# Optimization experiments

Hardware: AMD Instinct MI355X
Metric: run time of the kernel (lower is better)

Reference implementation:

```python
import jax, jax.numpy as jnp
import numpy as np

N0, N1, N2 = 400000, 100000, 25000   # nodes per scale (finest -> coarsest)
E0, E1, E2 = 1600000, 400000, 100000
HID, OUT = 64, 2
STATIC_D, DYN_D = 6, 10
K = 3  # filter-matrix polynomial order
NUM_SCALES = 3


def setup_inputs() -> dict:
    key = jax.random.key(0)
    ks = jax.random.split(key, 20)
    def nrm(k, shape, scale=1.0):
        return jax.random.normal(k, shape, dtype=jnp.float32) * scale
    Ntot = N0 + N1 + N2
    inp = {}
    inp["static_features"] = nrm(ks[0], (Ntot, STATIC_D))
    inp["dynamic_features"] = nrm(ks[1], (Ntot, DYN_D))
    Es, Ns = [E0, E1, E2], [N0, N1, N2]
    for i in range(NUM_SCALES):
        inp[f"edge_index{i}"] = jax.random.randint(ks[2 + i], (2, Es[i]), 0, Ns[i], dtype=jnp.int32)
        inp[f"edge_attr{i}"] = jax.random.uniform(ks[5 + i], (Es[i],), dtype=jnp.float32)
    inp["pool_idx1"] = jax.random.randint(ks[8], (N1,), 0, N0, dtype=jnp.int32)
    inp["pool_idx2"] = jax.random.randint(ks[9], (N2,), 0, N0, dtype=jnp.int32)
    fin = STATIC_D + DYN_D
    inp["enc_W1"] = nrm(ks[10], (fin, HID), 1.0 / np.sqrt(fin))
    inp["enc_b1"] = jnp.zeros((HID,), jnp.float32)
    inp["enc_W2"] = nrm(ks[11], (HID, HID), 1.0 / np.sqrt(HID))
    inp["enc_b2"] = jnp.zeros((HID,), jnp.float32)
    inp["enc_prelu"] = jnp.float32(0.25)
    inp["gcn_W"] = nrm(ks[12], (NUM_SCALES, HID, HID), 1.0 / np.sqrt(HID))
    inp["gcn_b"] = jnp.zeros((NUM_SCALES, HID), jnp.float32)
    inp["filter_matrix"] = jnp.ones((NUM_SCALES, K), jnp.float32)
    inp["dec_W1"] = nrm(ks[13], (HID, HID), 1.0 / np.sqrt(HID))
    inp["dec_b1"] = jnp.zeros((HID,), jnp.float32)
    inp["dec_W2"] = nrm(ks[14], (HID, OUT), 1.0 / np.sqrt(HID))
    inp["dec_b2"] = jnp.zeros((OUT,), jnp.float32)
    inp["dec_prelu"] = jnp.float32(0.25)
    return inp


def prelu(x, a):
    return jnp.where(x > 0, x, a * x)


def gcn_conv(x, W, b, src, dst, ew, n):
    # PyG GCNConv: linear, then symmetric-normalized propagation with self loops (weight 1), then bias.
    h = x @ W
    deg = jnp.zeros((n,), x.dtype).at[dst].add(ew) + 1.0  # +1 for self loop
    dinv = jax.lax.rsqrt(deg)
    norm = dinv[src] * ew * dinv[dst]                      # [E]
    out = jnp.zeros_like(h).at[dst].add(norm[:, None] * h[src])
    out = out + h * (dinv * dinv)[:, None]                 # self-loop term: 1/deg
    return out + b


def scatter_mean(x, idx, n):
    cnt = jnp.zeros((n,), x.dtype).at[idx].add(1.0)
    s = jnp.zeros((n, x.shape[1]), x.dtype).at[idx].add(x)
    return s / jnp.maximum(cnt, 1.0)[:, None]


def reference(static_features, dynamic_features, edge_index0, edge_attr0,
              edge_index1, edge_attr1, edge_index2, edge_attr2,
              pool_idx1, pool_idx2,
              enc_W1, enc_b1, enc_W2, enc_b2, enc_prelu,
              gcn_W, gcn_b, filter_matrix,
              dec_W1, dec_b1, dec_W2, dec_b2, dec_prelu):
    # Encoder MLP (prelu after every layer, shared prelu param per MLP)
    x = jnp.concatenate([static_features, dynamic_features], -1)
    x = prelu(x @ enc_W1 + enc_b1, enc_prelu)
    x = prelu(x @ enc_W2 + enc_b2, enc_prelu)

    # Split into scales (node_ptr is static)
    ptr = [0, N0, N0 + N1, N0 + N1 + N2]
    xs = [x[ptr[i]:ptr[i + 1]] for i in range(NUM_SCALES)]
    eis = [edge_index0, edge_index1, edge_index2]
    eas = [edge_attr0, edge_attr1, edge_attr2]
    Ns = [N0, N1, N2]

    # MSGNN layers: K repeated (conv -> tanh), mixed by filter_matrix
    outs = []
    for i in range(NUM_SCALES):
        src, dst = eis[i][0], eis[i][1]
        h = xs[i]
        acc = jnp.zeros_like(h)
        for k in range(K):
            h = jnp.tanh(gcn_conv(h, gcn_W[i], gcn_b[i], src, dst, eas[i], Ns[i]))
            acc = acc + filter_matrix[i, k] * h
        outs.append(acc)

    # Skip-connection pooling: scatter-mean coarse scales onto finest scale
    fin = outs[0]
    fin = fin + scatter_mean(outs[1], pool_idx1, N0)
    fin = fin + scatter_mean(outs[2], pool_idx2, N0)

    # Decoder MLP
    y = prelu(fin @ dec_W1 + dec_b1, dec_prelu)
    y = prelu(y @ dec_W2 + dec_b2, dec_prelu)
    return y
```

## Files before the change

kernel.cpp:

```cpp
#include <hip/hip_runtime.h>
#include <hip/hip_bf16.h>

typedef __hip_bfloat16 bf16;
typedef short  bf16x8  __attribute__((ext_vector_type(8)));
typedef __bf16 bf16x8n __attribute__((ext_vector_type(8)));
typedef float  f32x4   __attribute__((ext_vector_type(4)));

constexpr int cN0 = 400000, cN1 = 100000, cN2 = 25000;
constexpr int cNTOT = cN0 + cN1 + cN2;
constexpr int cE0 = 1600000, cE1 = 400000, cE2 = 100000;

static __device__ __forceinline__ float b2f(bf16 x) { return __bfloat162float(x); }

static __device__ __forceinline__ short f2bf_rtne(float f) {
    unsigned u = __float_as_uint(f);
    u = (u + 0x7fffu + ((u >> 16) & 1u)) >> 16;
    return (short)u;
}
static __device__ __forceinline__ void split2(float x, short& h, short& l) {
    unsigned u = __float_as_uint(x);
    h = (short)(u >> 16);
    l = f2bf_rtne(x - __uint_as_float(u & 0xffff0000u));
}

static __device__ __forceinline__ f32x4 mfma16(bf16x8 a, bf16x8 b, f32x4 c) {
    return __builtin_amdgcn_mfma_f32_16x16x32_bf16((bf16x8n)a, (bf16x8n)b, c, 0, 0, 0);
}

static __device__ __forceinline__ void pack_a8(const float* s8, bf16x8& ah, bf16x8& al) {
    float4 v0 = ((const float4*)s8)[0];
    float4 v1 = ((const float4*)s8)[1];
    float xx[8] = {v0.x, v0.y, v0.z, v0.w, v1.x, v1.y, v1.z, v1.w};
#pragma unroll
    for (int j = 0; j < 8; j++) { short h, l; split2(xx[j], h, l); ah[j] = h; al[j] = l; }
}

static __device__ __forceinline__ void pack_b8(const float* __restrict__ W, int ldn,
                                               int kbase, int col, int kmax,
                                               bf16x8& bh, bf16x8& bl) {
#pragma unroll
    for (int j = 0; j < 8; j++) {
        int k = kbase + j;
        float w = (k < kmax) ? W[(size_t)k * ldn + col] : 0.f;
        short h, l; split2(w, h, l); bh[j] = h; bl[j] = l;
    }
}

__global__ __launch_bounds__(256, 2)
void enc_kernel(const float* __restrict__ stat, const float* __restrict__ dyn,
                const float* __restrict__ W1, const float* __restrict__ b1,
                const float* __restrict__ W2, const float* __restrict__ b2,
                const float* __restrict__ pa, bf16* __restrict__ X, int nn)
{
    __shared__ float sF[4][16 * 20];
    __shared__ float sH[4][16 * 68];
    const int lane = threadIdx.x & 63;
    const int slot = threadIdx.x >> 6;
    const int r = lane & 15, g4 = lane >> 4;
    const int wid = blockIdx.x * (blockDim.x >> 6) + slot;
    const int nw  = gridDim.x * (blockDim.x >> 6);

    bf16x8 B1h[4], B1l[4], B2h[2][4], B2l[2][4];
#pragma unroll
    for (int nb = 0; nb < 4; nb++)
        pack_b8(W1, 64, g4 * 8, nb * 16 + r, 16, B1h[nb], B1l[nb]);
#pragma unroll
    for (int s = 0; s < 2; s++)
#pragma unroll
        for (int nb = 0; nb < 4; nb++)
            pack_b8(W2, 64, s * 32 + g4 * 8, nb * 16 + r, 64, B2h[s][nb], B2l[s][nb]);
    float bc1[4], bc2[4];
#pragma unroll
    for (int nb = 0; nb < 4; nb++) { bc1[nb] = b1[nb * 16 + r]; bc2[nb] = b2[nb * 16 + r]; }
    const float a = pa[0];
    float* F = sF[slot];
    float* H = sH[slot];
    const int ntile = (nn + 15) >> 4;

    for (int tt = wid; tt < ntile; tt += nw) {
        const int n0 = tt << 4;
        const int nv = min(16, nn - n0);
        for (int t = lane; t < nv * 6; t += 64)
            F[(t / 6) * 20 + (t % 6)] = stat[(size_t)n0 * 6 + t];
        for (int t = lane; t < nv * 10; t += 64)
            F[(t / 10) * 20 + 6 + (t % 10)] = dyn[(size_t)n0 * 10 + t];
        __builtin_amdgcn_wave_barrier();

        f32x4 C1[4];
#pragma unroll
        for (int nb = 0; nb < 4; nb++) C1[nb] = (f32x4){bc1[nb], bc1[nb], bc1[nb], bc1[nb]};
        bf16x8 ah, al;
        if (g4 < 2) pack_a8(F + r * 20 + g4 * 8, ah, al);
        else        { ah = (bf16x8)(short)0; al = (bf16x8)(short)0; }
#pragma unroll
        for (int nb = 0; nb < 4; nb++) {
            C1[nb] = mfma16(ah, B1h[nb], C1[nb]);
            C1[nb] = mfma16(ah, B1l[nb], C1[nb]);
            C1[nb] = mfma16(al, B1h[nb], C1[nb]);
        }
#pragma unroll
        for (int nb = 0; nb < 4; nb++)
#pragma unroll
            for (int q = 0; q < 4; q++) {
                float v = C1[nb][q];
                v = v > 0.f ? v : a * v;
                H[(g4 * 4 + q) * 68 + nb * 16 + r] = v;
            }
        __builtin_amdgcn_wave_barrier();

        f32x4 C2[4];
#pragma unroll
        for (int nb = 0; nb < 4; nb++) C2[nb] = (f32x4){bc2[nb], bc2[nb], bc2[nb], bc2[nb]};
#pragma unroll
        for (int s = 0; s < 2; s++) {
            bf16x8 a2h, a2l;
            pack_a8(H + r * 68 + s * 32 + g4 * 8, a2h, a2l);
#pragma unroll
            for (int nb = 0; nb < 4; nb++) {
                C2[nb] = mfma16(a2h, B2h[s][nb], C2[nb]);
                C2[nb] = mfma16(a2h, B2l[s][nb], C2[nb]);
                C2[nb] = mfma16(a2l, B2h[s][nb], C2[nb]);
            }
        }
#pragma unroll
        for (int nb = 0; nb < 4; nb++)
#pragma unroll
            for (int q = 0; q < 4; q++) {
                float v = C2[nb][q];
                v = v > 0.f ? v : a * v;
                const int row = g4 * 4 + q;
                if (row < nv)
                    X[(size_t)(n0 + row) * 64 + nb * 16 + r] = __float2bfloat16(v);
            }
        __builtin_amdgcn_wave_barrier();
    }
}

__global__ void zint_kernel(int* p, int n)   { int t = blockIdx.x * 256 + threadIdx.x; if (t < n) p[t] = 0; }
__global__ void fill1_kernel(float* p, int n){ int t = blockIdx.x * 256 + threadIdx.x; if (t < n) p[t] = 1.f; }
__global__ void degacc_kernel(const int* __restrict__ dst, const float* __restrict__ ew,
                              float* __restrict__ deg, int ne)
{
    int e = blockIdx.x * 256 + threadIdx.x;
    if (e < ne) unsafeAtomicAdd(&deg[dst[e]], ew[e]);
}
__global__ void rsqrt_kernel(float* p, int n){ int t = blockIdx.x * 256 + threadIdx.x; if (t < n) p[t] = rsqrtf(p[t]); }
__global__ void cnt_edge_kernel(const int* __restrict__ dst, int* __restrict__ cnt, int ne)
{
    int e = blockIdx.x * 256 + threadIdx.x;
    if (e < ne) atomicAdd(&cnt[dst[e]], 1);
}

__global__ void scan_blk_kernel(const int* __restrict__ cnt, int* __restrict__ base,
                                int* __restrict__ bsum, int n)
{
    __shared__ int s[256];
    const int tid = threadIdx.x;
    const int t = blockIdx.x * 256 + tid;
    int v = (t < n) ? cnt[t] : 0;
    s[tid] = v;
    __syncthreads();
#pragma unroll
    for (int d = 1; d < 256; d <<= 1) {
        int u = (tid >= d) ? s[tid - d] : 0;
        __syncthreads();
        s[tid] += u;
        __syncthreads();
    }
    if (t < n) base[t] = s[tid] - v;
    if (tid == 255) bsum[blockIdx.x] = s[255];
}
__global__ void scan_top_kernel(int* __restrict__ bsum, int nb)
{
    __shared__ int s[256];
    __shared__ int carry;
    const int tid = threadIdx.x;
    if (tid == 0) carry = 0;
    __syncthreads();
    for (int c0 = 0; c0 < nb; c0 += 256) {
        const int t = c0 + tid;
        int v = (t < nb) ? bsum[t] : 0;
        s[tid] = v;
        __syncthreads();
#pragma unroll
        for (int d = 1; d < 256; d <<= 1) {
            int u = (tid >= d) ? s[tid - d] : 0;
            __syncthreads();
            s[tid] += u;
            __syncthreads();
        }
        if (t < nb) bsum[t] = carry + s[tid] - v;
        __syncthreads();
        if (tid == 255) carry += s[255];
        __syncthreads();
    }
}
__global__ void scan_add_kernel(int* __restrict__ base, const int* __restrict__ bsum,
                                int* __restrict__ cur, int n)
{
    const int t = blockIdx.x * 256 + threadIdx.x;
    if (t < n) { int b = base[t] + bsum[blockIdx.x]; base[t] = b; cur[t] = b; }
}

__global__ void grab_kernel(const int* __restrict__ cnt, int* __restrict__ base,
                            int* __restrict__ cur, int* __restrict__ gc, int n)
{
    int t = blockIdx.x * 256 + threadIdx.x;
    if (t < n) { int b = atomicAdd(gc, cnt[t]); base[t] = b; cur[t] = b; }
}
__global__ void fill_edge_kernel(const int* __restrict__ src, const int* __restrict__ dst,
                                 const float* __restrict__ ew, const float* __restrict__ dinv,
                                 int* __restrict__ cur, int* __restrict__ srcp,
                                 bf16* __restrict__ normp, int ne)
{
    int e = blockIdx.x * 256 + threadIdx.x;
    if (e >= ne) return;
    int d = dst[e], s = src[e];
    int pos = atomicAdd(&cur[d], 1);
    srcp[pos]  = s;
    normp[pos] = __float2bfloat16(dinv[s] * ew[e] * dinv[d]);
}
__global__ void cnt_idx_kernel(const int* __restrict__ idx, int* __restrict__ cnt, int n)
{
    int j = blockIdx.x * 256 + threadIdx.x;
    if (j < n) atomicAdd(&cnt[idx[j]], 1);
}
__global__ void fill_idx_kernel(const int* __restrict__ idx, int* __restrict__ cur,
                                int* __restrict__ jp, int n)
{
    int j = blockIdx.x * 256 + threadIdx.x;
    if (j >= n) return;
    int pos = atomicAdd(&cur[idx[j]], 1);
    jp[pos] = j;
}

__global__ __launch_bounds__(256, 3)
void fused_conv_kernel(const int* __restrict__ base,
                       const int* __restrict__ srcp, const bf16* __restrict__ normp,
                       const bf16* __restrict__ h_in, bf16* __restrict__ h_out,
                       const float* __restrict__ dinv,
                       const float* __restrict__ W, int woff,
                       const float* __restrict__ bias, int boff,
                       const float* __restrict__ filt, int foff,
                       int first, int store_h, float* __restrict__ acc,
                       int nn, int ne)
{
    __shared__ float sb[4][16 * 68];
    const int lane = threadIdx.x & 63;
    const int slot = threadIdx.x >> 6;
    const int r = lane & 15, g4 = lane >> 4;
    const int wid  = blockIdx.x * (blockDim.x >> 6) + slot;
    const int nw   = gridDim.x * (blockDim.x >> 6);

    bf16x8 Bh[2][4], Bl[2][4];
#pragma unroll
    for (int s = 0; s < 2; s++)
#pragma unroll
        for (int nb = 0; nb < 4; nb++)
            pack_b8(W + woff, 64, s * 32 + g4 * 8, nb * 16 + r, 64, Bh[s][nb], Bl[s][nb]);
    float bc[4];
#pragma unroll
    for (int nb = 0; nb < 4; nb++) bc[nb] = bias[boff + nb * 16 + r];
    const float fc = filt[foff];
    float* sbrow = sb[slot];
    const int ngrp = (nn + 15) >> 4;

    for (int grp = wid; grp < ngrp; grp += nw) {
        const int n0 = grp << 4;
        const int idx = n0 + lane;
        int rpl = 0;
        if (lane <= 16) rpl = (idx < nn) ? base[idx] : ne;
        const int rp0 = __shfl(rpl, 0);
        const int rpG = __shfl(rpl, 16);

        int cur = 0;
        int rnext = __shfl(rpl, 1);
        float g = 0.f;

        for (int eb = rp0; eb < rpG; eb += 64) {
            const int cc = min(64, rpG - eb);
            int sv = 0; float nv = 0.f;
            if (lane < cc) {
                sv = srcp[eb + lane];
                nv = b2f(normp[eb + lane]);
            }
            for (int j = 0; j < cc; j += 8) {
                float p[8], m[8];
#pragma unroll
                for (int t = 0; t < 8; t++) {
                    const int jt = min(j + t, cc - 1);
                    const int st = __shfl(sv, jt);
                    const float mt = __shfl(nv, jt);
                    m[t] = (j + t < cc) ? mt : 0.f;
                    p[t] = b2f(h_in[(size_t)st * 64 + lane]);
                }
#pragma unroll
                for (int t = 0; t < 8; t++) {
                    const int je = eb + j + t;
                    while (je >= rnext) {
                        sbrow[cur * 68 + lane] = g;
                        g = 0.f;
                        cur++;
                        rnext = (cur < 16) ? __shfl(rpl, cur + 1) : 0x7fffffff;
                    }
                    g += m[t] * p[t];
                }
            }
        }
        while (cur < 16) {
            sbrow[cur * 68 + lane] = g;
            g = 0.f;
            cur++;
        }
        __builtin_amdgcn_wave_barrier();

        const int nv16 = min(16, nn - n0);
        for (int i = 0; i < nv16; i++) {
            const int n_i = n0 + i;
            const float di = dinv[n_i];
            sbrow[i * 68 + lane] += b2f(h_in[(size_t)n_i * 64 + lane]) * di * di;
        }
        __builtin_amdgcn_wave_barrier();

        f32x4 C[4];
#pragma unroll
        for (int nb = 0; nb < 4; nb++) C[nb] = (f32x4){bc[nb], bc[nb], bc[nb], bc[nb]};
#pragma unroll
        for (int s = 0; s < 2; s++) {
            bf16x8 ah, al;
            pack_a8(sbrow + r * 68 + s * 32 + g4 * 8, ah, al);
#pragma unroll
            for (int nb = 0; nb < 4; nb++) {
                C[nb] = mfma16(ah, Bh[s][nb], C[nb]);
                C[nb] = mfma16(ah, Bl[s][nb], C[nb]);
                C[nb] = mfma16(al, Bh[s][nb], C[nb]);
            }
        }
#pragma unroll
        for (int nb = 0; nb < 4; nb++)
#pragma unroll
            for (int q = 0; q < 4; q++) {
                const int row = g4 * 4 + q;
                if (row < nv16) {
                    const float sv_ = C[nb][q];
                    const float e = __expf(2.f * sv_);
                    const float h = 1.f - 2.f * __builtin_amdgcn_rcpf(e + 1.f);
                    const size_t ai = (size_t)(n0 + row) * 64 + nb * 16 + r;
                    if (store_h) h_out[ai] = __float2bfloat16(h);
                    acc[ai] = (first ? 0.f : acc[ai]) + fc * h;
                }
            }
        __builtin_amdgcn_wave_barrier();
    }
}

__global__ void pool_gather_kernel(const int* __restrict__ base, const int* __restrict__ cnt,
                                   const int* __restrict__ jp, const float* __restrict__ accc,
                                   float* __restrict__ fin, int nn)
{
    const int lane = threadIdx.x & 63;
    const int n = blockIdx.x * (blockDim.x >> 6) + (threadIdx.x >> 6);
    if (n >= nn) return;
    const int m = cnt[n];
    if (m == 0) return;
    const int bs = base[n];
    float s = 0.f;
    for (int t = bs; t < bs + m; t++) {
        int j = jp[t];
        s += accc[(size_t)j * 64 + lane];
    }
    fin[(size_t)n * 64 + lane] += s / (float)m;
}

__global__ __launch_bounds__(256, 3)
void dec_kernel(const float* __restrict__ fin,
                const float* __restrict__ W1, const float* __restrict__ b1,
                const float* __restrict__ W2, const float* __restrict__ b2,
                const float* __restrict__ pa, float* __restrict__ out, int nn)
{
    const int lane = threadIdx.x & 63;
    const int r = lane & 15, g4 = lane >> 4;
    const int wid = blockIdx.x * (blockDim.x >> 6) + (threadIdx.x >> 6);
    const int nw  = gridDim.x * (blockDim.x >> 6);

    bf16x8 Wh[2][4], Wl[2][4];
#pragma unroll
    for (int s = 0; s < 2; s++)
#pragma unroll
        for (int nb = 0; nb < 4; nb++)
            pack_b8(W1, 64, s * 32 + g4 * 8, nb * 16 + r, 64, Wh[s][nb], Wl[s][nb]);
    float bc[4], w20[4], w21[4];
#pragma unroll
    for (int nb = 0; nb < 4; nb++) {
        bc[nb]  = b1[nb * 16 + r];
        w20[nb] = W2[(nb * 16 + r) * 2 + 0];
        w21[nb] = W2[(nb * 16 + r) * 2 + 1];
    }
    const float bb20 = b2[0], bb21 = b2[1];
    const float a = pa[0];
    const int ntile = (nn + 15) >> 4;

    for (int tt = wid; tt < ntile; tt += nw) {
        const int n0 = tt << 4;
        f32x4 C[4];
#pragma unroll
        for (int nb = 0; nb < 4; nb++) C[nb] = (f32x4){bc[nb], bc[nb], bc[nb], bc[nb]};
#pragma unroll
        for (int s = 0; s < 2; s++) {
            bf16x8 ah, al;
            pack_a8(fin + (size_t)(n0 + r) * 64 + s * 32 + g4 * 8, ah, al);
#pragma unroll
            for (int nb = 0; nb < 4; nb++) {
                C[nb] = mfma16(ah, Wh[s][nb], C[nb]);
                C[nb] = mfma16(ah, Wl[s][nb], C[nb]);
                C[nb] = mfma16(al, Wh[s][nb], C[nb]);
            }
        }
#pragma unroll
        for (int q = 0; q < 4; q++) {
            float p0 = 0.f, p1 = 0.f;
#pragma unroll
            for (int nb = 0; nb < 4; nb++) {
                float y = C[nb][q];
                y = y > 0.f ? y : a * y;
                p0 += y * w20[nb]; p1 += y * w21[nb];
            }
            p0 += __shfl_xor(p0, 1); p1 += __shfl_xor(p1, 1);
            p0 += __shfl_xor(p0, 2); p1 += __shfl_xor(p1, 2);
            p0 += __shfl_xor(p0, 4); p1 += __shfl_xor(p1, 4);
            p0 += __shfl_xor(p0, 8); p1 += __shfl_xor(p1, 8);
            if (r == 0) {
                const int node = n0 + g4 * 4 + q;
                if (node < nn) {
                    float o0 = p0 + bb20; o0 = o0 > 0.f ? o0 : a * o0;
                    float o1 = p1 + bb21; o1 = o1 > 0.f ? o1 : a * o1;
                    ((float2*)out)[node] = make_float2(o0, o1);
                }
            }
        }
    }
}

extern "C" void kernel_launch(void* const* d_in, const int* in_sizes, int n_in,
                              void* d_out, int out_size, void* d_ws, size_t ws_size,
                              hipStream_t stream)
{
    const float* stat = (const float*)d_in[0];
    const float* dyn  = (const float*)d_in[1];
    const int*   ei[3]   = {(const int*)d_in[2], (const int*)d_in[4], (const int*)d_in[6]};
    const float* ea[3]   = {(const float*)d_in[3], (const float*)d_in[5], (const float*)d_in[7]};
    const int*   pidx[2] = {(const int*)d_in[8], (const int*)d_in[9]};
    const float* encW1 = (const float*)d_in[10]; const float* encb1 = (const float*)d_in[11];
    const float* encW2 = (const float*)d_in[12]; const float* encb2 = (const float*)d_in[13];
    const float* encpa = (const float*)d_in[14];
    const float* gW    = (const float*)d_in[15]; const float* gbias = (const float*)d_in[16];
    const float* filt  = (const float*)d_in[17];
    const float* dW1   = (const float*)d_in[18]; const float* db1   = (const float*)d_in[19];
    const float* dW2   = (const float*)d_in[20]; const float* db2   = (const float*)d_in[21];
    const float* dpa   = (const float*)d_in[22];

    auto al = [](size_t x) { return (x + 255) & ~(size_t)255; };
    char* w = (char*)d_ws;
    size_t off = 0;
    bf16* X    = (bf16*)(w + off); off += al((size_t)cNTOT * 64 * 2);
    bf16* HB   = (bf16*)(w + off); off += al((size_t)cN0 * 64 * 2);
    float* FIN = (float*)(w + off); off += al((size_t)cN0 * 64 * 4);
    float* ACCC= (float*)(w + off); off += al((size_t)cN1 * 64 * 4);
    float* DINV= (float*)(w + off); off += al((size_t)cN0 * 4);
    int* CNTI  = (int*)(w + off);  off += al((size_t)cN0 * 4);
    int* BASE  = (int*)(w + off);  off += al((size_t)cN0 * 4);
    int* CUR   = (int*)(w + off);  off += al((size_t)cN0 * 4);
    int* SRCP  = (int*)(w + off);  off += al((size_t)cE0 * 4);
    bf16* NORMP= (bf16*)(w + off); off += al((size_t)cE0 * 2);
    int* JP    = (int*)(w + off);  off += al((size_t)cN1 * 4);
    int* GC    = (int*)(w + off);  off += 256;
    int* BSUM  = (int*)(w + off);  off += al((size_t)2048 * 4);

    const int Ns[3]  = {cN0, cN1, cN2};
    const int Es[3]  = {cE0, cE1, cE2};
    const int ptr[3] = {0, cN0, cN0 + cN1};
#define NB(x) (((x) + 255) / 256)

    enc_kernel<<<4096, 256, 0, stream>>>(stat, dyn, encW1, encb1, encW2, encb2, encpa, X, cNTOT);

    for (int i = 0; i < 3; i++) {
        const int* srcp_in = ei[i];
        const int* dstp    = ei[i] + Es[i];
        fill1_kernel <<<NB(Ns[i]), 256, 0, stream>>>(DINV, Ns[i]);
        degacc_kernel<<<NB(Es[i]), 256, 0, stream>>>(dstp, ea[i], DINV, Es[i]);
        rsqrt_kernel <<<NB(Ns[i]), 256, 0, stream>>>(DINV, Ns[i]);
        zint_kernel    <<<NB(Ns[i]), 256, 0, stream>>>(CNTI, Ns[i]);
        cnt_edge_kernel<<<NB(Es[i]), 256, 0, stream>>>(dstp, CNTI, Es[i]);
        scan_blk_kernel<<<NB(Ns[i]), 256, 0, stream>>>(CNTI, BASE, BSUM, Ns[i]);
        scan_top_kernel<<<1, 256, 0, stream>>>(BSUM, NB(Ns[i]));
        scan_add_kernel<<<NB(Ns[i]), 256, 0, stream>>>(BASE, BSUM, CUR, Ns[i]);
        fill_edge_kernel<<<NB(Es[i]), 256, 0, stream>>>(srcp_in, dstp, ea[i], DINV, CUR, SRCP, NORMP, Es[i]);

        bf16* ping = X + (size_t)ptr[i] * 64;
        bf16* pong = HB;
        float* acc_i = (i == 0) ? FIN : ACCC;
        for (int k = 0; k < 3; k++) {
            bf16* hin  = (k & 1) ? pong : ping;
            bf16* hout = (k & 1) ? ping : pong;
            fused_conv_kernel<<<4096, 256, 0, stream>>>(BASE, SRCP, NORMP,
                hin, hout, DINV, gW, i * 4096, gbias, i * 64,
                filt, i * 3 + k, (k == 0) ? 1 : 0, (k < 2) ? 1 : 0, acc_i, Ns[i], Es[i]);
        }
        if (i >= 1) {
            int nj = (i == 1) ? cN1 : cN2;
            const int* pp = pidx[i - 1];
            zint_kernel    <<<NB(cN0), 256, 0, stream>>>(CNTI, cN0);
            zint_kernel    <<<1, 256, 0, stream>>>(GC, 1);
            cnt_idx_kernel <<<NB(nj), 256, 0, stream>>>(pp, CNTI, nj);
            grab_kernel    <<<NB(cN0), 256, 0, stream>>>(CNTI, BASE, CUR, GC, cN0);
            fill_idx_kernel<<<NB(nj), 256, 0, stream>>>(pp, CUR, JP, nj);
            pool_gather_kernel<<<(cN0 + 3) / 4, 256, 0, stream>>>(BASE, CNTI, JP, ACCC, FIN, cN0);
        }
    }
    dec_kernel<<<4096, 256, 0, stream>>>(FIN, dW1, db1, dW2, db2, dpa, (float*)d_out, cN0);
#undef NB
}
```

Before: 1.552 ms.

## Restructure edge aggregation into 4-node lane groups and fuse preprocessing kernels

The gather-aggregate loop in the fused conv kernel now splits the wave into four 16-lane groups. Each group handles four destination nodes and each lane loads 4 bf16 features with one 8-byte load, replacing the old scheme of one feature per lane per edge with a shared serial segment walk. The self-loop term is vectorised per row. Preprocessing kernels are fused: init of dinv and counts, degree plus count atomics, rsqrt folded into the block scan, and the two zeroing kernels merged. The conv grid is sized to the number of node groups, which cuts launch count and idle waves but adds some lane divergence from per-group segment flushing.

```diff
diff --git a/kernel.cpp b/kernel.cpp
--- a/kernel.cpp
+++ b/kernel.cpp
@@ -11,6 +11,8 @@
 constexpr int cE0 = 1600000, cE1 = 400000, cE2 = 100000;
 
 static __device__ __forceinline__ float b2f(bf16 x) { return __bfloat162float(x); }
+static __device__ __forceinline__ float bflo(unsigned u) { return __uint_as_float(u << 16); }
+static __device__ __forceinline__ float bfhi(unsigned u) { return __uint_as_float(u & 0xffff0000u); }
 
 static __device__ __forceinline__ short f2bf_rtne(float f) {
     unsigned u = __float_as_uint(f);
@@ -136,23 +138,24 @@
     }
 }
 
-__global__ void zint_kernel(int* p, int n)   { int t = blockIdx.x * 256 + threadIdx.x; if (t < n) p[t] = 0; }
-__global__ void fill1_kernel(float* p, int n){ int t = blockIdx.x * 256 + threadIdx.x; if (t < n) p[t] = 1.f; }
-__global__ void degacc_kernel(const int* __restrict__ dst, const float* __restrict__ ew,
-                              float* __restrict__ deg, int ne)
+__global__ void init_scale_kernel(float* dinv, int* cnti, int n)
+{
+    int t = blockIdx.x * 256 + threadIdx.x;
+    if (t < n) { dinv[t] = 1.f; cnti[t] = 0; }
+}
+__global__ void edge_deg_cnt_kernel(const int* __restrict__ dst, const float* __restrict__ ew,
+                                    float* __restrict__ deg, int* __restrict__ cnt, int ne)
 {
     int e = blockIdx.x * 256 + threadIdx.x;
-    if (e < ne) unsafeAtomicAdd(&deg[dst[e]], ew[e]);
-}
-__global__ void rsqrt_kernel(float* p, int n){ int t = blockIdx.x * 256 + threadIdx.x; if (t < n) p[t] = rsqrtf(p[t]); }
-__global__ void cnt_edge_kernel(const int* __restrict__ dst, int* __restrict__ cnt, int ne)
-{
-    int e = blockIdx.x * 256 + threadIdx.x;
-    if (e < ne) atomicAdd(&cnt[dst[e]], 1);
+    if (e < ne) {
+        int d = dst[e];
+        unsafeAtomicAdd(&deg[d], ew[e]);
+        atomicAdd(&cnt[d], 1);
+    }
 }
 
 __global__ void scan_blk_kernel(const int* __restrict__ cnt, int* __restrict__ base,
-                                int* __restrict__ bsum, int n)
+                                int* __restrict__ bsum, float* __restrict__ dinv, int n)
 {
     __shared__ int s[256];
     const int tid = threadIdx.x;
@@ -167,7 +170,10 @@
         s[tid] += u;
         __syncthreads();
     }
-    if (t < n) base[t] = s[tid] - v;
+    if (t < n) {
+        base[t] = s[tid] - v;
+        dinv[t] = rsqrtf(dinv[t]);
+    }
     if (tid == 255) bsum[blockIdx.x] = s[255];
 }
 __global__ void scan_top_kernel(int* __restrict__ bsum, int nb)
@@ -220,6 +226,12 @@
     srcp[pos]  = s;
     normp[pos] = __float2bfloat16(dinv[s] * ew[e] * dinv[d]);
 }
+__global__ void zint2_kernel(int* __restrict__ p, int* __restrict__ gc, int n)
+{
+    int t = blockIdx.x * 256 + threadIdx.x;
+    if (t < n) p[t] = 0;
+    if (t == 0 && blockIdx.x == 0) gc[0] = 0;
+}
 __global__ void cnt_idx_kernel(const int* __restrict__ idx, int* __restrict__ cnt, int n)
 {
     int j = blockIdx.x * 256 + threadIdx.x;
@@ -267,61 +279,79 @@
 
     for (int grp = wid; grp < ngrp; grp += nw) {
         const int n0 = grp << 4;
-        const int idx = n0 + lane;
         int rpl = 0;
-        if (lane <= 16) rpl = (idx < nn) ? base[idx] : ne;
-        const int rp0 = __shfl(rpl, 0);
-        const int rpG = __shfl(rpl, 16);
-
-        int cur = 0;
-        int rnext = __shfl(rpl, 1);
-        float g = 0.f;
-
-        for (int eb = rp0; eb < rpG; eb += 64) {
-            const int cc = min(64, rpG - eb);
-            int sv = 0; float nv = 0.f;
-            if (lane < cc) {
-                sv = srcp[eb + lane];
-                nv = b2f(normp[eb + lane]);
-            }
-            for (int j = 0; j < cc; j += 8) {
-                float p[8], m[8];
-#pragma unroll
-                for (int t = 0; t < 8; t++) {
-                    const int jt = min(j + t, cc - 1);
-                    const int st = __shfl(sv, jt);
-                    const float mt = __shfl(nv, jt);
-                    m[t] = (j + t < cc) ? mt : 0.f;
-                    p[t] = b2f(h_in[(size_t)st * 64 + lane]);
-                }
-#pragma unroll
-                for (int t = 0; t < 8; t++) {
-                    const int je = eb + j + t;
-                    while (je >= rnext) {
-                        sbrow[cur * 68 + lane] = g;
-                        g = 0.f;
-                        cur++;
-                        rnext = (cur < 16) ? __shfl(rpl, cur + 1) : 0x7fffffff;
-                    }
-                    g += m[t] * p[t];
-                }
-            }
-        }
-        while (cur < 16) {
-            sbrow[cur * 68 + lane] = g;
-            g = 0.f;
-            cur++;
-        }
+        if (lane <= 16) rpl = (n0 + lane < nn) ? base[n0 + lane] : ne;
+        const int b4 = g4 << 2;
+        const int q0 = __shfl(rpl, b4);
+        const int q1 = __shfl(rpl, b4 + 1);
+        const int q2 = __shfl(rpl, b4 + 2);
+        const int q3 = __shfl(rpl, b4 + 3);
+        const int q4 = __shfl(rpl, b4 + 4);
+
+        int   curl  = 0;
+        int   rnext = q1;
+        float g0 = 0.f, g1 = 0.f, g2 = 0.f, g3 = 0.f;
+        auto flush = [&]() {
+            *(float4*)(sbrow + (b4 + curl) * 68 + (r << 2)) = make_float4(g0, g1, g2, g3);
+            g0 = g1 = g2 = g3 = 0.f;
+            curl++;
+            rnext = (curl == 1) ? q2 : (curl == 2) ? q3 : (curl == 3) ? q4 : 0x7fffffff;
+        };
+
+        for (int eb = q0; eb < q4; eb += 16) {
+            const int ei_ = min(eb + r, q4 - 1);
+            int   sv = srcp[ei_];
+            float nv = (eb + r < q4) ? b2f(normp[ei_]) : 0.f;
+#pragma unroll
+            for (int t = 0; t < 16; t += 4) {
+                const int bidx = (g4 << 4) + t;
+                int   s0 = __shfl(sv, bidx),     s1 = __shfl(sv, bidx + 1);
+                int   s2 = __shfl(sv, bidx + 2), s3 = __shfl(sv, bidx + 3);
+                float m0 = __shfl(nv, bidx),     m1 = __shfl(nv, bidx + 1);
+                float m2 = __shfl(nv, bidx + 2), m3 = __shfl(nv, bidx + 3);
+                uint2 p0 = *(const uint2*)(h_in + ((size_t)s0 << 6) + (r << 2));
+                uint2 p1 = *(const uint2*)(h_in + ((size_t)s1 << 6) + (r << 2));
+                uint2 p2 = *(const uint2*)(h_in + ((size_t)s2 << 6) + (r << 2));
+                uint2 p3 = *(const uint2*)(h_in + ((size_t)s3 << 6) + (r << 2));
+                while (eb + t     >= rnext) flush();
+                g0 += m0 * bflo(p0.x); g1 += m0 * bfhi(p0.x);
+                g2 += m0 * bflo(p0.y); g3 += m0 * bfhi(p0.y);
+                while (eb + t + 1 >= rnext) flush();
+                g0 += m1 * bflo(p1.x); g1 += m1 * bfhi(p1.x);
+                g2 += m1 * bflo(p1.y); g3 += m1 * bfhi(p1.y);
+                while (eb + t + 2 >= rnext) flush();
+                g0 += m2 * bflo(p2.x); g1 += m2 * bfhi(p2.x);
+                g2 += m2 * bflo(p2.y); g3 += m2 * bfhi(p2.y);
+                while (eb + t + 3 >= rnext) flush();
+                g0 += m3 * bflo(p3.x); g1 += m3 * bfhi(p3.x);
+                g2 += m3 * bflo(p3.y); g3 += m3 * bfhi(p3.y);
+            }
+        }
+        while (curl < 4) flush();
         __builtin_amdgcn_wave_barrier();
 
+        {
+            const int node = n0 + r;
+            const int ncl = min(node, nn - 1);
+            float di = dinv[ncl];
+            di = (node < nn) ? di * di : 0.f;
+            float* rowp = sbrow + r * 68 + (g4 << 4);
+#pragma unroll
+            for (int hh = 0; hh < 2; hh++) {
+                uint4 hv = *(const uint4*)(h_in + ((size_t)ncl << 6) + (g4 << 4) + hh * 8);
+                float4 f0 = *(float4*)(rowp + hh * 8);
+                float4 f1 = *(float4*)(rowp + hh * 8 + 4);
+                f0.x += di * bflo(hv.x); f0.y += di * bfhi(hv.x);
+                f0.z += di * bflo(hv.y); f0.w += di * bfhi(hv.y);
+                f1.x += di * bflo(hv.z); f1.y += di * bfhi(hv.z);
+                f1.z += di * bflo(hv.w); f1.w += di * bfhi(hv.w);
+                *(float4*)(rowp + hh * 8)     = f0;
+                *(float4*)(rowp + hh * 8 + 4) = f1;
+            }
+        }
+        __builtin_amdgcn_wave_barrier();
+
         const int nv16 = min(16, nn - n0);
-        for (int i = 0; i < nv16; i++) {
-            const int n_i = n0 + i;
-            const float di = dinv[n_i];
-            sbrow[i * 68 + lane] += b2f(h_in[(size_t)n_i * 64 + lane]) * di * di;
-        }
-        __builtin_amdgcn_wave_barrier();
-
         f32x4 C[4];
 #pragma unroll
         for (int nb = 0; nb < 4; nb++) C[nb] = (f32x4){bc[nb], bc[nb], bc[nb], bc[nb]};
@@ -486,31 +516,29 @@
     for (int i = 0; i < 3; i++) {
         const int* srcp_in = ei[i];
         const int* dstp    = ei[i] + Es[i];
-        fill1_kernel <<<NB(Ns[i]), 256, 0, stream>>>(DINV, Ns[i]);
-        degacc_kernel<<<NB(Es[i]), 256, 0, stream>>>(dstp, ea[i], DINV, Es[i]);
-        rsqrt_kernel <<<NB(Ns[i]), 256, 0, stream>>>(DINV, Ns[i]);
-        zint_kernel    <<<NB(Ns[i]), 256, 0, stream>>>(CNTI, Ns[i]);
-        cnt_edge_kernel<<<NB(Es[i]), 256, 0, stream>>>(dstp, CNTI, Es[i]);
-        scan_blk_kernel<<<NB(Ns[i]), 256, 0, stream>>>(CNTI, BASE, BSUM, Ns[i]);
-        scan_top_kernel<<<1, 256, 0, stream>>>(BSUM, NB(Ns[i]));
-        scan_add_kernel<<<NB(Ns[i]), 256, 0, stream>>>(BASE, BSUM, CUR, Ns[i]);
-        fill_edge_kernel<<<NB(Es[i]), 256, 0, stream>>>(srcp_in, dstp, ea[i], DINV, CUR, SRCP, NORMP, Es[i]);
+        init_scale_kernel  <<<NB(Ns[i]), 256, 0, stream>>>(DINV, CNTI, Ns[i]);
+        edge_deg_cnt_kernel<<<NB(Es[i]), 256, 0, stream>>>(dstp, ea[i], DINV, CNTI, Es[i]);
+        scan_blk_kernel    <<<NB(Ns[i]), 256, 0, stream>>>(CNTI, BASE, BSUM, DINV, Ns[i]);
+        scan_top_kernel    <<<1, 256, 0, stream>>>(BSUM, NB(Ns[i]));
+        scan_add_kernel    <<<NB(Ns[i]), 256, 0, stream>>>(BASE, BSUM, CUR, Ns[i]);
+        fill_edge_kernel   <<<NB(Es[i]), 256, 0, stream>>>(srcp_in, dstp, ea[i], DINV, CUR, SRCP, NORMP, Es[i]);
 
         bf16* ping = X + (size_t)ptr[i] * 64;
         bf16* pong = HB;
         float* acc_i = (i == 0) ? FIN : ACCC;
+        const int ngrp = (Ns[i] + 15) / 16;
+        const int cblk = min(4096, (ngrp + 3) / 4);
         for (int k = 0; k < 3; k++) {
             bf16* hin  = (k & 1) ? pong : ping;
             bf16* hout = (k & 1) ? ping : pong;
-            fused_conv_kernel<<<4096, 256, 0, stream>>>(BASE, SRCP, NORMP,
+            fused_conv_kernel<<<cblk, 256, 0, stream>>>(BASE, SRCP, NORMP,
                 hin, hout, DINV, gW, i * 4096, gbias, i * 64,
                 filt, i * 3 + k, (k == 0) ? 1 : 0, (k < 2) ? 1 : 0, acc_i, Ns[i], Es[i]);
         }
         if (i >= 1) {
             int nj = (i == 1) ? cN1 : cN2;
             const int* pp = pidx[i - 1];
-            zint_kernel    <<<NB(cN0), 256, 0, stream>>>(CNTI, cN0);
-            zint_kernel    <<<1, 256, 0, stream>>>(GC, 1);
+            zint2_kernel   <<<NB(cN0), 256, 0, stream>>>(CNTI, GC, cN0);
             cnt_idx_kernel <<<NB(nj), 256, 0, stream>>>(pp, CNTI, nj);
             grab_kernel    <<<NB(cN0), 256, 0, stream>>>(CNTI, BASE, CUR, GC, cN0);
             fill_idx_kernel<<<NB(nj), 256, 0, stream>>>(pp, CUR, JP, nj);
```

Measured after the change: 1.396 ms. 1.11x faster.
